# Kernel optimization log

Measured on AMD Instinct MI355X. Metric: run time of the kernel, lower is better.

Reference implementation:

```python
import jax, jax.numpy as jnp
import numpy as np

B, L, C, R = 8192, 49, 512, 128  # L = 7*7 hardcoded in module
H = W = 7


def _conv2d(x, w, b, pad):
    # x: (B, Cin, H, W), w: (Cout, Cin, k, k)
    y = jax.lax.conv_general_dilated(
        x, w, window_strides=(1, 1), padding=[(pad, pad), (pad, pad)],
        dimension_numbers=("NCHW", "OIHW", "NCHW"))
    return y + b[None, :, None, None]


def _star_relu(x, scale, bias):
    r = jnp.maximum(x, 0.0)
    return scale * (r * r) + bias


def setup_inputs() -> dict:
    key = jax.random.key(0)
    ks = jax.random.split(key, 12)
    s = 0.05
    return {
        "x": jax.random.normal(ks[0], (B, L, C), jnp.float32),
        "g_reduce_w": jax.random.normal(ks[1], (R, C), jnp.float32) * s,
        "l_reduce_w": jax.random.normal(ks[2], (R, C), jnp.float32) * s,
        "conv3_w": jax.random.normal(ks[3], (R // 2, R // 2, 3, 3), jnp.float32) * s,
        "conv3_b": jax.random.normal(ks[4], (R // 2,), jnp.float32) * s,
        "conv5_w": jax.random.normal(ks[5], (R - R // 2, R - R // 2, 5, 5), jnp.float32) * s,
        "conv5_b": jax.random.normal(ks[6], (R - R // 2,), jnp.float32) * s,
        "channel_w": jax.random.normal(ks[7], (C, R), jnp.float32) * s,
        "channel_b": jax.random.normal(ks[8], (C,), jnp.float32) * s,
        "spatial_w": jax.random.normal(ks[9], (1, 3 * R), jnp.float32) * s,
        "spatial_b": jax.random.normal(ks[10], (1,), jnp.float32) * s,
        "star_scale": jnp.ones((1,), jnp.float32),
        "star_bias": jnp.zeros((1,), jnp.float32),
    }


def reference(x, g_reduce_w, l_reduce_w, conv3_w, conv3_b, conv5_w, conv5_b,
              channel_w, channel_b, spatial_w, spatial_b, star_scale, star_bias):
    # x: (B, L, C) with L = 49 (7x7)
    # Global dual pooling over spatial (== over L)
    x_max = jnp.max(x, axis=1)   # (B, C)
    x_avg = jnp.mean(x, axis=1)  # (B, C)
    # g_reduce 1x1 conv (no bias) + StarReLU
    g1 = _star_relu(x_max @ g_reduce_w.T, star_scale, star_bias)  # (B, R)
    g2 = _star_relu(x_avg @ g_reduce_w.T, star_scale, star_bias)  # (B, R)
    # Local branch: 1x1 reduce -> HybConv2d (split 3x3 / 5x5) -> StarReLU
    x_img = x.transpose(0, 2, 1).reshape(B, C, H, W)
    x_l = jnp.einsum("bchw,rc->brhw", x_img, l_reduce_w)  # (B, R, 7, 7)
    xl1, xl2 = x_l[:, :R // 2], x_l[:, R // 2:]
    y1 = _conv2d(xl1, conv3_w, conv3_b, pad=1)
    y2 = _conv2d(xl2, conv5_w, conv5_b, pad=2)
    x_l = _star_relu(jnp.concatenate([y1, y2], axis=1), star_scale, star_bias)
    x_l = x_l.reshape(B, R, L).transpose(0, 2, 1)  # (B, L, R)
    # Channel gate: Linear(R->C) applied to each pooled branch, summed
    c_aggr = jax.nn.sigmoid((g1 @ channel_w.T + channel_b)
                            + (g2 @ channel_w.T + channel_b))  # (B, C)
    # Spatial gate: concat [x_l, g1 broadcast, g2 broadcast] -> Linear(3R->1)
    g1b = jnp.broadcast_to(g1[:, None, :], (B, L, R))
    g2b = jnp.broadcast_to(g2[:, None, :], (B, L, R))
    s_cat = jnp.concatenate([x_l, g1b, g2b], axis=-1)  # (B, L, 3R)
    s_aggr = jax.nn.sigmoid(jnp.einsum("blk,ok->blo", s_cat, spatial_w) + spatial_b)  # (B, L, 1)
    aggr = c_aggr[:, None, :] * s_aggr  # (B, L, C)
    return x * aggr
```

## Files before the change

### kernel.cpp

```cpp
#include <hip/hip_runtime.h>
#include <math.h>

#define B_ 8192
#define L_ 49
#define C_ 512
#define R_ 128

typedef short   bf16x8 __attribute__((ext_vector_type(8)));
typedef unsigned short u16x8 __attribute__((ext_vector_type(8)));
typedef float   f32x4  __attribute__((ext_vector_type(4)));

#define WS_LWF   0
#define WS_WB3F  65536
#define WS_WB5F  102400
#define WS_GWF   204800
#define WS_CWF   270336

#define SM_XB    0
#define SM_XLP   25088
#define SM_MAXB  58000
#define SM_SUMF  62096
#define SM_GA    70288
#define SM_G     71312
#define SM_HB    72336
#define SM_CA    72592
#define SM_SPW   74640
#define SM_SP    76688
#define SM_GDOT  76944
#define SM_TOT   76960

#define XLP_N    16456
#define DBIAS    3264

__device__ __forceinline__ float bf2f(unsigned short u) {
    union { float f; unsigned int i; } v; v.i = ((unsigned int)u) << 16; return v.f;
}
__device__ __forceinline__ unsigned short f2bf(float f) {
    union { float f; unsigned int i; } v; v.f = f;
    unsigned int r = v.i + 0x7fffu + ((v.i >> 16) & 1u);
    return (unsigned short)(r >> 16);
}
__device__ __forceinline__ unsigned int pkbf(float a, float b) {
    unsigned int r;
    asm("v_cvt_pk_bf16_f32 %0, %1, %2" : "=v"(r) : "v"(a), "v"(b));
    return r;
}
__device__ __forceinline__ float star_relu(float x, float sc, float bi) {
    float r = fmaxf(x, 0.f);
    return sc * r * r + bi;
}
__device__ __forceinline__ float sigmoidf_(float x) {
    return 1.f / (1.f + __expf(-x));
}
__device__ __forceinline__ int prowf(int lp) {
    int pi = lp / 7, pj = lp - pi * 7;
    return (pi + 2) * 11 + (pj + 2);
}

__global__ void cvt_weights(const float* __restrict__ lw, const float* __restrict__ w3,
                            const float* __restrict__ w5, const float* __restrict__ gw,
                            const float* __restrict__ cw, unsigned short* __restrict__ ws)
{
    int t = blockIdx.x * blockDim.x + threadIdx.x;
    int stride = gridDim.x * blockDim.x;
    for (int i = t; i < 65536; i += stride) {
        int j = i & 7, lane = (i >> 3) & 63, ks = (i >> 9) & 15, nt = i >> 13;
        int n = nt * 16 + (lane & 15);
        int k = ks * 32 + (lane >> 4) * 8 + j;
        ws[WS_LWF + i] = f2bf(lw[n * 512 + k]);
        ws[WS_GWF + i] = f2bf(gw[n * 512 + k]);
    }
    for (int i = t; i < 65536; i += stride) {
        int j = i & 7, lane = (i >> 3) & 63, ks = (i >> 9) & 3, nf = i >> 11;
        int c = nf * 16 + (lane & 15);
        int k = ks * 32 + (lane >> 4) * 8 + j;
        ws[WS_CWF + i] = f2bf(cw[c * 128 + k]);
    }
    for (int i = t; i < 36864; i += stride) {
        int j = i & 7, lane = (i >> 3) & 63, ks = (i >> 9) & 1, f = (i >> 10) & 3, tap = i >> 12;
        int oc = f * 16 + (lane & 15);
        int ic = ks * 32 + (lane >> 4) * 8 + j;
        ws[WS_WB3F + i] = f2bf(w3[(oc * 64 + ic) * 9 + tap]);
    }
    for (int i = t; i < 102400; i += stride) {
        int j = i & 7, lane = (i >> 3) & 63, ks = (i >> 9) & 1, f = (i >> 10) & 3, tap = i >> 12;
        int oc = f * 16 + (lane & 15);
        int ic = ks * 32 + (lane >> 4) * 8 + j;
        ws[WS_WB5F + i] = f2bf(w5[(oc * 64 + ic) * 25 + tap]);
    }
}

template <int NTAP, int KD, int PAD, int COLBASE>
__device__ __forceinline__ void conv_mfma(const unsigned short* __restrict__ s_xlp,
                                          const unsigned short* __restrict__ wtbf,
                                          int m16, int kg, int ln, int f, f32x4 C[4])
{
    int base[4];
    #pragma unroll
    for (int mf = 0; mf < 4; ++mf) {
        int lp = min(mf * 16 + m16, 48);
        base[mf] = prowf(lp) * 136 + COLBASE + kg * 8 - DBIAS;
    }
    #pragma unroll
    for (int tap = 0; tap < NTAP; ++tap) {
        const int doff = ((tap / KD - PAD) * 11 + (tap % KD - PAD)) * 136 + DBIAS;
        #pragma unroll
        for (int ks = 0; ks < 2; ++ks) {
            bf16x8 bb = *(const bf16x8*)(wtbf + ((tap * 4 + f) * 2 + ks) * 512 + ln * 8);
            #pragma unroll
            for (int mf = 0; mf < 4; ++mf) {
                bf16x8 a = *(const bf16x8*)&s_xlp[base[mf] + doff + ks * 32];
                C[mf] = __builtin_amdgcn_mfma_f32_16x16x32_bf16(a, bb, C[mf], 0, 0, 0);
            }
        }
    }
}

__global__ __launch_bounds__(512, 4)
void mafn_fused(const float* __restrict__ x,
                const float* __restrict__ b3, const float* __restrict__ b5,
                const float* __restrict__ cb, const float* __restrict__ sw,
                const float* __restrict__ sb, const float* __restrict__ ssc,
                const float* __restrict__ sbi,
                const unsigned short* __restrict__ ws,
                float* __restrict__ out)
{
    __shared__ __align__(16) unsigned char smem[SM_TOT];
    unsigned short* s_xb   = (unsigned short*)(smem + SM_XB);
    unsigned short* s_xlp  = (unsigned short*)(smem + SM_XLP);
    unsigned short* s_maxb = (unsigned short*)(smem + SM_MAXB);
    float*          s_sumf = (float*)(smem + SM_SUMF);
    unsigned short* s_ga   = (unsigned short*)(smem + SM_GA);
    float*          s_g    = (float*)(smem + SM_G);
    unsigned short* s_hb   = (unsigned short*)(smem + SM_HB);
    float*          s_ca   = (float*)(smem + SM_CA);
    float*          s_spw  = (float*)(smem + SM_SPW);
    float*          s_sp   = (float*)(smem + SM_SP);
    float*          s_gdot = (float*)(smem + SM_GDOT);

    const int b = blockIdx.x, t = threadIdx.x;
    const int wv = t >> 6, ln = t & 63;
    const int m16 = ln & 15, kg = ln >> 4;
    const float scale = ssc[0], sbias = sbi[0];

    const unsigned short* lwf  = ws + WS_LWF;
    const unsigned short* wb3f = ws + WS_WB3F;
    const unsigned short* wb5f = ws + WS_WB5F;
    const unsigned short* gwf  = ws + WS_GWF;
    const unsigned short* cwf  = ws + WS_CWF;

    f32x4 accA[4];
    f32x4 accG;
    {
        const f32x4 z = {0.f, 0.f, 0.f, 0.f};
        #pragma unroll
        for (int mf = 0; mf < 4; ++mf) accA[mf] = z;
        accG = z;
    }

    for (int i = t; i < XLP_N / 2; i += 512) ((unsigned int*)s_xlp)[i] = 0;

    const int l0 = wv * 6;
    const int nl = (wv < 7) ? 6 : 7;

    #pragma unroll 1
    for (int h = 0; h < 2; ++h) {
        {
            const float4* x4 = (const float4*)(x + (size_t)b * (L_ * C_)) + h * 64;
            float4 mx = {-3.4e38f, -3.4e38f, -3.4e38f, -3.4e38f};
            float4 sm = {0.f, 0.f, 0.f, 0.f};
            for (int li = 0; li < nl; ++li) {
                int l = l0 + li;
                float4 v = x4[l * 128 + ln];
                mx.x = fmaxf(mx.x, v.x); mx.y = fmaxf(mx.y, v.y);
                mx.z = fmaxf(mx.z, v.z); mx.w = fmaxf(mx.w, v.w);
                sm.x += v.x; sm.y += v.y; sm.z += v.z; sm.w += v.w;
                uint2 p; p.x = pkbf(v.x, v.y); p.y = pkbf(v.z, v.w);
                int chunk = (ln >> 1) ^ (l & 7);
                *(uint2*)&s_xb[l * 256 + chunk * 8 + (ln & 1) * 4] = p;
            }
            uint2 pm; pm.x = pkbf(mx.x, mx.y); pm.y = pkbf(mx.z, mx.w);
            *(uint2*)&s_maxb[wv * 256 + ln * 4] = pm;
            *(float4*)&s_sumf[wv * 256 + ln * 4] = sm;
        }
        __syncthreads();

        {
            if (t < 256) {
                int c = t;
                float m = bf2f(s_maxb[c]);
                #pragma unroll
                for (int i = 1; i < 8; ++i) m = fmaxf(m, bf2f(s_maxb[i * 256 + c]));
                s_ga[c] = f2bf(m);
            } else {
                int c = t - 256;
                float s = 0.f;
                #pragma unroll
                for (int i = 0; i < 8; ++i) s += s_sumf[i * 256 + c];
                s_ga[256 + c] = f2bf(s * (1.f / 49.f));
            }
        }
        __syncthreads();

        {
            int rowA[4];
            #pragma unroll
            for (int mf = 0; mf < 4; ++mf) rowA[mf] = min(mf * 16 + m16, 48);
            #pragma unroll 2
            for (int ks = 0; ks < 8; ++ks) {
                bf16x8 bb = *(const bf16x8*)(lwf + (wv * 16 + h * 8 + ks) * 512 + ln * 8);
                #pragma unroll
                for (int mf = 0; mf < 4; ++mf) {
                    int chunk = (ks * 4 + kg) ^ (rowA[mf] & 7);
                    bf16x8 a = *(const bf16x8*)&s_xb[rowA[mf] * 256 + chunk * 8];
                    accA[mf] = __builtin_amdgcn_mfma_f32_16x16x32_bf16(a, bb, accA[mf], 0, 0, 0);
                }
            }
            const bf16x8 zz = {0,0,0,0,0,0,0,0};
            #pragma unroll 4
            for (int ks = 0; ks < 8; ++ks) {
                bf16x8 a = (m16 < 2) ? *(const bf16x8*)&s_ga[m16 * 256 + ks * 32 + kg * 8] : zz;
                bf16x8 bb = *(const bf16x8*)(gwf + (wv * 16 + h * 8 + ks) * 512 + ln * 8);
                accG = __builtin_amdgcn_mfma_f32_16x16x32_bf16(a, bb, accG, 0, 0, 0);
            }
        }
        __syncthreads();
    }

    {
        const int n = wv * 16 + m16;
        #pragma unroll
        for (int mf = 0; mf < 4; ++mf) {
            #pragma unroll
            for (int rp = 0; rp < 2; ++rp) {
                unsigned int u = pkbf(accA[mf][rp * 2], accA[mf][rp * 2 + 1]);
                int lp0 = mf * 16 + kg * 4 + rp * 2;
                if (lp0 < 49)     s_xlp[prowf(lp0) * 136 + n]     = (unsigned short)u;
                if (lp0 + 1 < 49) s_xlp[prowf(lp0 + 1) * 136 + n] = (unsigned short)(u >> 16);
            }
        }
        if (kg == 0) {
            float g1v = star_relu(accG[0], scale, sbias);
            float g2v = star_relu(accG[1], scale, sbias);
            s_g[n] = g1v;
            s_g[128 + n] = g2v;
            s_hb[n] = f2bf(g1v + g2v);
        }
    }
    __syncthreads();

    const int f_ = wv & 3;
    const int oc_ = f_ * 16 + m16;
    {
        f32x4 C[4];
        const f32x4 z = {0.f, 0.f, 0.f, 0.f};
        #pragma unroll
        for (int mf = 0; mf < 4; ++mf) C[mf] = z;

        if (wv < 4) {
            conv_mfma<25, 5, 2, 64>(s_xlp, wb5f, m16, kg, ln, f_, C);
        } else {
            conv_mfma< 9, 3, 1,  0>(s_xlp, wb3f, m16, kg, ln, f_, C);
            bf16x8 aH[4];
            #pragma unroll
            for (int ks = 0; ks < 4; ++ks) {
                bf16x8 tt = {0,0,0,0,0,0,0,0};
                if (m16 == 0) tt = *(const bf16x8*)&s_hb[ks * 32 + kg * 8];
                aH[ks] = tt;
            }
            const int nf0 = (wv - 4) * 8;
            #pragma unroll 2
            for (int q = 0; q < 8; ++q) {
                int nf = nf0 + q;
                f32x4 acc = z;
                #pragma unroll
                for (int ks = 0; ks < 4; ++ks) {
                    bf16x8 bb = *(const bf16x8*)(cwf + ((nf * 4 + ks) * 64 + ln) * 8);
                    acc = __builtin_amdgcn_mfma_f32_16x16x32_bf16(aH[ks], bb, acc, 0, 0, 0);
                }
                if (kg == 0) {
                    int c = nf * 16 + m16;
                    s_ca[c] = sigmoidf_(acc[0] + 2.f * cb[c]);
                }
            }
            if (wv == 7) {
                float p = s_g[ln] * sw[128 + ln] + s_g[128 + ln] * sw[256 + ln]
                        + s_g[ln + 64] * sw[128 + ln + 64] + s_g[128 + ln + 64] * sw[256 + ln + 64];
                #pragma unroll
                for (int off = 32; off > 0; off >>= 1) p += __shfl_xor(p, off);
                if (ln == 0) s_gdot[0] = p;
            }
        }

        const bool is5 = (wv < 4);
        const int ch = is5 ? 64 + oc_ : oc_;
        const float bias = is5 ? b5[oc_] : b3[oc_];
        const float sww = sw[ch];
        #pragma unroll
        for (int mf = 0; mf < 4; ++mf) {
            #pragma unroll
            for (int rg = 0; rg < 4; ++rg) {
                int lp = mf * 16 + kg * 4 + rg;
                float v = (lp < 49) ? star_relu(C[mf][rg] + bias, scale, sbias) * sww : 0.f;
                v += __shfl_xor(v, 1);
                v += __shfl_xor(v, 2);
                v += __shfl_xor(v, 4);
                v += __shfl_xor(v, 8);
                if (m16 == 0 && lp < 49) s_spw[wv * 64 + lp] = v;
            }
        }
    }
    __syncthreads();

    if (t < 49) {
        float s = s_gdot[0] + sb[0];
        #pragma unroll
        for (int w = 0; w < 8; ++w) s += s_spw[w * 64 + t];
        s_sp[t] = sigmoidf_(s);
    }
    __syncthreads();

    {
        const float4* x4 = (const float4*)(x + (size_t)b * (L_ * C_));
        float4* o4 = (float4*)(out + (size_t)b * (L_ * C_));
        const float4* ca4 = (const float4*)s_ca;
        for (int i = t; i < 49 * 128; i += 512) {
            int l = i >> 7, c4 = i & 127;
            float4 xv = x4[i];
            float g = s_sp[l];
            float4 cv = ca4[c4];
            float4 ov;
            ov.x = xv.x * cv.x * g;
            ov.y = xv.y * cv.y * g;
            ov.z = xv.z * cv.z * g;
            ov.w = xv.w * cv.w * g;
            o4[i] = ov;
        }
    }
}

extern "C" void kernel_launch(void* const* d_in, const int* in_sizes, int n_in,
                              void* d_out, int out_size, void* d_ws, size_t ws_size,
                              hipStream_t stream) {
    (void)in_sizes; (void)n_in; (void)ws_size; (void)out_size;
    const float* x    = (const float*)d_in[0];
    const float* g_w  = (const float*)d_in[1];
    const float* l_w  = (const float*)d_in[2];
    const float* w3   = (const float*)d_in[3];
    const float* b3   = (const float*)d_in[4];
    const float* w5   = (const float*)d_in[5];
    const float* b5   = (const float*)d_in[6];
    const float* cw   = (const float*)d_in[7];
    const float* cb   = (const float*)d_in[8];
    const float* sw   = (const float*)d_in[9];
    const float* sb   = (const float*)d_in[10];
    const float* ssc  = (const float*)d_in[11];
    const float* sbi  = (const float*)d_in[12];
    float* outp = (float*)d_out;
    unsigned short* ws = (unsigned short*)d_ws;

    cvt_weights<<<dim3(512), dim3(256), 0, stream>>>(l_w, w3, w5, g_w, cw, ws);
    mafn_fused<<<dim3(B_), dim3(512), 0, stream>>>(
        x, b3, b5, cb, sw, sb, ssc, sbi, ws, outp);
}
```

Before: 708.0 us.

## Rebalance MFMA work across waves with 2-wide N tiles and split 5x5 taps

Each wave now computes two N-fragments per A-fragment load in the reduce GEMM and the convolutions, so every LDS A read feeds two MFMAs. The 5x5 conv is split by tap range across wave pairs, with partial sums exchanged through shared memory. The channel-gate GEMM moves to waves 6-7 so the conv and gate work are spread more evenly. This adds an extra barrier and a shared-memory partial-sum exchange, raises register pressure, and makes the gate-branch GEMM run on only four waves.

```diff
diff --git a/kernel.cpp b/kernel.cpp
--- a/kernel.cpp
+++ b/kernel.cpp
@@ -31,6 +31,7 @@
 
 #define XLP_N    16456
 #define DBIAS    3264
+#define PARTN    1617
 
 __device__ __forceinline__ float bf2f(unsigned short u) {
     union { float f; unsigned int i; } v; v.i = ((unsigned int)u) << 16; return v.f;
@@ -90,10 +91,10 @@
     }
 }
 
-template <int NTAP, int KD, int PAD, int COLBASE>
-__device__ __forceinline__ void conv_mfma(const unsigned short* __restrict__ s_xlp,
-                                          const unsigned short* __restrict__ wtbf,
-                                          int m16, int kg, int ln, int f, f32x4 C[4])
+template <int KD, int PAD, int COLBASE, int T0, int T1>
+__device__ __forceinline__ void conv2(const unsigned short* __restrict__ s_xlp,
+                                      const unsigned short* __restrict__ wtbf,
+                                      int m16, int kg, int ln, int nf0, f32x4 C[4][2])
 {
     int base[4];
     #pragma unroll
@@ -102,15 +103,17 @@
         base[mf] = prowf(lp) * 136 + COLBASE + kg * 8 - DBIAS;
     }
     #pragma unroll
-    for (int tap = 0; tap < NTAP; ++tap) {
+    for (int tap = T0; tap < T1; ++tap) {
         const int doff = ((tap / KD - PAD) * 11 + (tap % KD - PAD)) * 136 + DBIAS;
         #pragma unroll
         for (int ks = 0; ks < 2; ++ks) {
-            bf16x8 bb = *(const bf16x8*)(wtbf + ((tap * 4 + f) * 2 + ks) * 512 + ln * 8);
+            bf16x8 bb0 = *(const bf16x8*)(wtbf + ((tap * 4 + nf0)     * 2 + ks) * 512 + ln * 8);
+            bf16x8 bb1 = *(const bf16x8*)(wtbf + ((tap * 4 + nf0 + 1) * 2 + ks) * 512 + ln * 8);
             #pragma unroll
             for (int mf = 0; mf < 4; ++mf) {
                 bf16x8 a = *(const bf16x8*)&s_xlp[base[mf] + doff + ks * 32];
-                C[mf] = __builtin_amdgcn_mfma_f32_16x16x32_bf16(a, bb, C[mf], 0, 0, 0);
+                C[mf][0] = __builtin_amdgcn_mfma_f32_16x16x32_bf16(a, bb0, C[mf][0], 0, 0, 0);
+                C[mf][1] = __builtin_amdgcn_mfma_f32_16x16x32_bf16(a, bb1, C[mf][1], 0, 0, 0);
             }
         }
     }
@@ -127,6 +130,7 @@
 {
     __shared__ __align__(16) unsigned char smem[SM_TOT];
     unsigned short* s_xb   = (unsigned short*)(smem + SM_XB);
+    float*          s_part = (float*)(smem + SM_XB);
     unsigned short* s_xlp  = (unsigned short*)(smem + SM_XLP);
     unsigned short* s_maxb = (unsigned short*)(smem + SM_MAXB);
     float*          s_sumf = (float*)(smem + SM_SUMF);
@@ -149,13 +153,15 @@
     const unsigned short* gwf  = ws + WS_GWF;
     const unsigned short* cwf  = ws + WS_CWF;
 
-    f32x4 accA[4];
-    f32x4 accG;
+    const int mfbase = (wv >= 4) ? 2 : 0;
+    const int nfp = (wv & 3) * 2;
+
+    f32x4 accA[2][2];
+    f32x4 accG[2];
     {
         const f32x4 z = {0.f, 0.f, 0.f, 0.f};
-        #pragma unroll
-        for (int mf = 0; mf < 4; ++mf) accA[mf] = z;
-        accG = z;
+        accA[0][0] = z; accA[0][1] = z; accA[1][0] = z; accA[1][1] = z;
+        accG[0] = z; accG[1] = z;
     }
 
     for (int i = t; i < XLP_N / 2; i += 512) ((unsigned int*)s_xlp)[i] = 0;
@@ -203,110 +209,171 @@
         __syncthreads();
 
         {
-            int rowA[4];
-            #pragma unroll
-            for (int mf = 0; mf < 4; ++mf) rowA[mf] = min(mf * 16 + m16, 48);
+            int rowA[2];
+            #pragma unroll
+            for (int mf2 = 0; mf2 < 2; ++mf2)
+                rowA[mf2] = min((mfbase + mf2) * 16 + m16, 48);
             #pragma unroll 2
             for (int ks = 0; ks < 8; ++ks) {
-                bf16x8 bb = *(const bf16x8*)(lwf + (wv * 16 + h * 8 + ks) * 512 + ln * 8);
+                bf16x8 bb0 = *(const bf16x8*)(lwf + ((nfp)     * 16 + h * 8 + ks) * 512 + ln * 8);
+                bf16x8 bb1 = *(const bf16x8*)(lwf + ((nfp + 1) * 16 + h * 8 + ks) * 512 + ln * 8);
                 #pragma unroll
-                for (int mf = 0; mf < 4; ++mf) {
-                    int chunk = (ks * 4 + kg) ^ (rowA[mf] & 7);
-                    bf16x8 a = *(const bf16x8*)&s_xb[rowA[mf] * 256 + chunk * 8];
-                    accA[mf] = __builtin_amdgcn_mfma_f32_16x16x32_bf16(a, bb, accA[mf], 0, 0, 0);
+                for (int mf2 = 0; mf2 < 2; ++mf2) {
+                    int chunk = (ks * 4 + kg) ^ (rowA[mf2] & 7);
+                    bf16x8 a = *(const bf16x8*)&s_xb[rowA[mf2] * 256 + chunk * 8];
+                    accA[mf2][0] = __builtin_amdgcn_mfma_f32_16x16x32_bf16(a, bb0, accA[mf2][0], 0, 0, 0);
+                    accA[mf2][1] = __builtin_amdgcn_mfma_f32_16x16x32_bf16(a, bb1, accA[mf2][1], 0, 0, 0);
                 }
             }
-            const bf16x8 zz = {0,0,0,0,0,0,0,0};
-            #pragma unroll 4
-            for (int ks = 0; ks < 8; ++ks) {
-                bf16x8 a = (m16 < 2) ? *(const bf16x8*)&s_ga[m16 * 256 + ks * 32 + kg * 8] : zz;
-                bf16x8 bb = *(const bf16x8*)(gwf + (wv * 16 + h * 8 + ks) * 512 + ln * 8);
-                accG = __builtin_amdgcn_mfma_f32_16x16x32_bf16(a, bb, accG, 0, 0, 0);
+            if (wv < 4) {
+                const bf16x8 zz = {0,0,0,0,0,0,0,0};
+                #pragma unroll 2
+                for (int ks = 0; ks < 8; ++ks) {
+                    bf16x8 a = (m16 < 2) ? *(const bf16x8*)&s_ga[m16 * 256 + ks * 32 + kg * 8] : zz;
+                    bf16x8 gb0 = *(const bf16x8*)(gwf + ((nfp)     * 16 + h * 8 + ks) * 512 + ln * 8);
+                    bf16x8 gb1 = *(const bf16x8*)(gwf + ((nfp + 1) * 16 + h * 8 + ks) * 512 + ln * 8);
+                    accG[0] = __builtin_amdgcn_mfma_f32_16x16x32_bf16(a, gb0, accG[0], 0, 0, 0);
+                    accG[1] = __builtin_amdgcn_mfma_f32_16x16x32_bf16(a, gb1, accG[1], 0, 0, 0);
+                }
             }
         }
         __syncthreads();
     }
 
     {
-        const int n = wv * 16 + m16;
-        #pragma unroll
-        for (int mf = 0; mf < 4; ++mf) {
-            #pragma unroll
-            for (int rp = 0; rp < 2; ++rp) {
-                unsigned int u = pkbf(accA[mf][rp * 2], accA[mf][rp * 2 + 1]);
-                int lp0 = mf * 16 + kg * 4 + rp * 2;
-                if (lp0 < 49)     s_xlp[prowf(lp0) * 136 + n]     = (unsigned short)u;
-                if (lp0 + 1 < 49) s_xlp[prowf(lp0 + 1) * 136 + n] = (unsigned short)(u >> 16);
-            }
-        }
-        if (kg == 0) {
-            float g1v = star_relu(accG[0], scale, sbias);
-            float g2v = star_relu(accG[1], scale, sbias);
-            s_g[n] = g1v;
-            s_g[128 + n] = g2v;
-            s_hb[n] = f2bf(g1v + g2v);
+        const int nb = nfp * 16 + m16;
+        #pragma unroll
+        for (int mf2 = 0; mf2 < 2; ++mf2) {
+            #pragma unroll
+            for (int q = 0; q < 2; ++q) {
+                #pragma unroll
+                for (int rp = 0; rp < 2; ++rp) {
+                    unsigned int u = pkbf(accA[mf2][q][rp * 2], accA[mf2][q][rp * 2 + 1]);
+                    int lp0 = (mfbase + mf2) * 16 + kg * 4 + rp * 2;
+                    if (lp0 < 49)     s_xlp[prowf(lp0) * 136 + nb + q * 16]     = (unsigned short)u;
+                    if (lp0 + 1 < 49) s_xlp[prowf(lp0 + 1) * 136 + nb + q * 16] = (unsigned short)(u >> 16);
+                }
+            }
+        }
+        if (wv < 4 && kg == 0) {
+            #pragma unroll
+            for (int q = 0; q < 2; ++q) {
+                int n = (nfp + q) * 16 + m16;
+                float g1v = star_relu(accG[q][0], scale, sbias);
+                float g2v = star_relu(accG[q][1], scale, sbias);
+                s_g[n] = g1v;
+                s_g[128 + n] = g2v;
+                s_hb[n] = f2bf(g1v + g2v);
+            }
         }
     }
     __syncthreads();
 
-    const int f_ = wv & 3;
-    const int oc_ = f_ * 16 + m16;
+    f32x4 C[4][2];
     {
-        f32x4 C[4];
         const f32x4 z = {0.f, 0.f, 0.f, 0.f};
         #pragma unroll
-        for (int mf = 0; mf < 4; ++mf) C[mf] = z;
-
-        if (wv < 4) {
-            conv_mfma<25, 5, 2, 64>(s_xlp, wb5f, m16, kg, ln, f_, C);
+        for (int mf = 0; mf < 4; ++mf) { C[mf][0] = z; C[mf][1] = z; }
+    }
+    const int nf0c = (wv < 4) ? (wv & 2) : ((wv - 4) * 2);
+    if (wv < 4) {
+        if ((wv & 1) == 0) {
+            conv2<5, 2, 64, 0, 13>(s_xlp, wb5f, m16, kg, ln, nf0c, C);
+            float* pp = s_part + (wv >> 1) * PARTN;
+            #pragma unroll
+            for (int mf = 0; mf < 4; ++mf) {
+                #pragma unroll
+                for (int q = 0; q < 2; ++q) {
+                    #pragma unroll
+                    for (int rg = 0; rg < 4; ++rg) {
+                        int lp = mf * 16 + kg * 4 + rg;
+                        if (lp < 49) pp[lp * 33 + q * 16 + m16] = C[mf][q][rg];
+                    }
+                }
+            }
         } else {
-            conv_mfma< 9, 3, 1,  0>(s_xlp, wb3f, m16, kg, ln, f_, C);
-            bf16x8 aH[4];
+            conv2<5, 2, 64, 13, 25>(s_xlp, wb5f, m16, kg, ln, nf0c, C);
+        }
+    } else if (wv < 6) {
+        conv2<3, 1, 0, 0, 9>(s_xlp, wb3f, m16, kg, ln, nf0c, C);
+    } else {
+        const f32x4 z = {0.f, 0.f, 0.f, 0.f};
+        bf16x8 aH[4];
+        #pragma unroll
+        for (int ks = 0; ks < 4; ++ks) {
+            bf16x8 tt = {0,0,0,0,0,0,0,0};
+            if (m16 == 0) tt = *(const bf16x8*)&s_hb[ks * 32 + kg * 8];
+            aH[ks] = tt;
+        }
+        const int nfb = (wv - 6) * 16;
+        #pragma unroll 2
+        for (int it = 0; it < 8; ++it) {
+            int nf0 = nfb + it * 2;
+            f32x4 a0 = z, a1 = z;
             #pragma unroll
             for (int ks = 0; ks < 4; ++ks) {
-                bf16x8 tt = {0,0,0,0,0,0,0,0};
-                if (m16 == 0) tt = *(const bf16x8*)&s_hb[ks * 32 + kg * 8];
-                aH[ks] = tt;
-            }
-            const int nf0 = (wv - 4) * 8;
-            #pragma unroll 2
-            for (int q = 0; q < 8; ++q) {
-                int nf = nf0 + q;
-                f32x4 acc = z;
-                #pragma unroll
-                for (int ks = 0; ks < 4; ++ks) {
-                    bf16x8 bb = *(const bf16x8*)(cwf + ((nf * 4 + ks) * 64 + ln) * 8);
-                    acc = __builtin_amdgcn_mfma_f32_16x16x32_bf16(aH[ks], bb, acc, 0, 0, 0);
-                }
-                if (kg == 0) {
-                    int c = nf * 16 + m16;
-                    s_ca[c] = sigmoidf_(acc[0] + 2.f * cb[c]);
-                }
-            }
-            if (wv == 7) {
-                float p = s_g[ln] * sw[128 + ln] + s_g[128 + ln] * sw[256 + ln]
-                        + s_g[ln + 64] * sw[128 + ln + 64] + s_g[128 + ln + 64] * sw[256 + ln + 64];
-                #pragma unroll
-                for (int off = 32; off > 0; off >>= 1) p += __shfl_xor(p, off);
-                if (ln == 0) s_gdot[0] = p;
-            }
-        }
-
-        const bool is5 = (wv < 4);
-        const int ch = is5 ? 64 + oc_ : oc_;
-        const float bias = is5 ? b5[oc_] : b3[oc_];
-        const float sww = sw[ch];
+                bf16x8 bb0 = *(const bf16x8*)(cwf + (((nf0)     * 4 + ks) * 64 + ln) * 8);
+                bf16x8 bb1 = *(const bf16x8*)(cwf + (((nf0 + 1) * 4 + ks) * 64 + ln) * 8);
+                a0 = __builtin_amdgcn_mfma_f32_16x16x32_bf16(aH[ks], bb0, a0, 0, 0, 0);
+                a1 = __builtin_amdgcn_mfma_f32_16x16x32_bf16(aH[ks], bb1, a1, 0, 0, 0);
+            }
+            if (kg == 0) {
+                int c0 = nf0 * 16 + m16;
+                s_ca[c0] = sigmoidf_(a0[0] + 2.f * cb[c0]);
+                int c1 = c0 + 16;
+                s_ca[c1] = sigmoidf_(a1[0] + 2.f * cb[c1]);
+            }
+        }
+        if (wv == 7) {
+            float p = s_g[ln] * sw[128 + ln] + s_g[128 + ln] * sw[256 + ln]
+                    + s_g[ln + 64] * sw[128 + ln + 64] + s_g[128 + ln + 64] * sw[256 + ln + 64];
+            #pragma unroll
+            for (int off = 32; off > 0; off >>= 1) p += __shfl_xor(p, off);
+            if (ln == 0) s_gdot[0] = p;
+        }
+    }
+    if (wv == 4 || wv == 5) {
+        const float bi0 = b3[nf0c * 16 + m16], bi1 = b3[(nf0c + 1) * 16 + m16];
+        const float sw0 = sw[nf0c * 16 + m16], sw1 = sw[(nf0c + 1) * 16 + m16];
         #pragma unroll
         for (int mf = 0; mf < 4; ++mf) {
             #pragma unroll
             for (int rg = 0; rg < 4; ++rg) {
                 int lp = mf * 16 + kg * 4 + rg;
-                float v = (lp < 49) ? star_relu(C[mf][rg] + bias, scale, sbias) * sww : 0.f;
+                float v = star_relu(C[mf][0][rg] + bi0, scale, sbias) * sw0
+                        + star_relu(C[mf][1][rg] + bi1, scale, sbias) * sw1;
+                v = (lp < 49) ? v : 0.f;
                 v += __shfl_xor(v, 1);
                 v += __shfl_xor(v, 2);
                 v += __shfl_xor(v, 4);
                 v += __shfl_xor(v, 8);
-                if (m16 == 0 && lp < 49) s_spw[wv * 64 + lp] = v;
+                if (m16 == 0 && lp < 49) s_spw[(wv - 2) * 64 + lp] = v;
+            }
+        }
+    }
+    __syncthreads();
+
+    if (wv == 1 || wv == 3) {
+        const float* pp = s_part + (wv >> 1) * PARTN;
+        const int oc0 = nf0c * 16 + m16, oc1 = oc0 + 16;
+        const float bi0 = b5[oc0], bi1 = b5[oc1];
+        const float sw0 = sw[64 + oc0], sw1 = sw[64 + oc1];
+        #pragma unroll
+        for (int mf = 0; mf < 4; ++mf) {
+            #pragma unroll
+            for (int rg = 0; rg < 4; ++rg) {
+                int lp = mf * 16 + kg * 4 + rg;
+                int lps = min(lp, 48);
+                float c0 = C[mf][0][rg] + pp[lps * 33 + m16];
+                float c1 = C[mf][1][rg] + pp[lps * 33 + 16 + m16];
+                float v = star_relu(c0 + bi0, scale, sbias) * sw0
+                        + star_relu(c1 + bi1, scale, sbias) * sw1;
+                v = (lp < 49) ? v : 0.f;
+                v += __shfl_xor(v, 1);
+                v += __shfl_xor(v, 2);
+                v += __shfl_xor(v, 4);
+                v += __shfl_xor(v, 8);
+                if (m16 == 0 && lp < 49) s_spw[(wv >> 1) * 64 + lp] = v;
             }
         }
     }
@@ -315,7 +382,7 @@
     if (t < 49) {
         float s = s_gdot[0] + sb[0];
         #pragma unroll
-        for (int w = 0; w < 8; ++w) s += s_spw[w * 64 + t];
+        for (int w = 0; w < 4; ++w) s += s_spw[w * 64 + t];
         s_sp[t] = sigmoidf_(s);
     }
     __syncthreads();
@@ -323,12 +390,12 @@
     {
         const float4* x4 = (const float4*)(x + (size_t)b * (L_ * C_));
         float4* o4 = (float4*)(out + (size_t)b * (L_ * C_));
-        const float4* ca4 = (const float4*)s_ca;
+        const int c4 = t & 127;
+        const float4 cv = *(const float4*)&s_ca[c4 * 4];
         for (int i = t; i < 49 * 128; i += 512) {
-            int l = i >> 7, c4 = i & 127;
+            int l = i >> 7;
             float4 xv = x4[i];
             float g = s_sp[l];
-            float4 cv = ca4[c4];
             float4 ov;
             ov.x = xv.x * cv.x * g;
             ov.y = xv.y * cv.y * g;
```

Result: slower. 756.8 us (+6.9%).
